# Kernel optimization log

Measured on AMD Instinct MI355X. Metric: run time of the kernel, lower is better.

The kernel has to match this reference:

```python
import jax, jax.numpy as jnp
import numpy as np

SEQ_LEN = 512
EMB_DIM = 2 * SEQ_LEN  # 1024
HIDDEN = 512
NUM_CLASSES = 10
BATCH = 256
VOCAB = 3


def setup_inputs() -> dict:
    key = jax.random.key(0)
    ks = jax.random.split(key, 16)
    def kaiming(k, shape, gain):
        fan_in = shape[0]
        return jax.random.normal(k, shape, dtype=jnp.float32) * (gain / np.sqrt(fan_in))
    tanh_g, sig_g, lin_g = np.sqrt(5.0 / 3.0), 1.0, 1.0
    return {
        "x": jax.random.randint(ks[0], (BATCH, SEQ_LEN), 0, VOCAB),
        "emb": jax.random.normal(ks[1], (VOCAB, EMB_DIM), dtype=jnp.float32),
        "W_gx": kaiming(ks[2], (EMB_DIM, HIDDEN), tanh_g),
        "W_gh": kaiming(ks[3], (HIDDEN, HIDDEN), tanh_g),
        "b_g": jnp.zeros((HIDDEN,), jnp.float32),
        "W_ix": kaiming(ks[4], (EMB_DIM, HIDDEN), sig_g),
        "W_ih": kaiming(ks[5], (HIDDEN, HIDDEN), sig_g),
        "b_i": jnp.zeros((HIDDEN,), jnp.float32),
        "W_fx": kaiming(ks[6], (EMB_DIM, HIDDEN), sig_g),
        "W_fh": kaiming(ks[7], (HIDDEN, HIDDEN), sig_g),
        "b_f": jnp.zeros((HIDDEN,), jnp.float32),
        "W_ox": kaiming(ks[8], (EMB_DIM, HIDDEN), sig_g),
        "W_oh": kaiming(ks[9], (HIDDEN, HIDDEN), sig_g),
        "b_o": jnp.zeros((HIDDEN,), jnp.float32),
        "W_ph": kaiming(ks[10], (HIDDEN, NUM_CLASSES), lin_g),
        "b_p": jnp.zeros((NUM_CLASSES,), jnp.float32),
    }


def reference(x, emb, W_gx, W_gh, b_g, W_ix, W_ih, b_i,
              W_fx, W_fh, b_f, W_ox, W_oh, b_o, W_ph, b_p):
    # Embed all tokens: [B, T, E]
    xe = emb[x]
    B = xe.shape[0]
    # Precompute input projections for all gates once: [T, B, 4H]
    Wx = jnp.concatenate([W_gx, W_ix, W_fx, W_ox], axis=1)  # [E, 4H]
    Wh = jnp.concatenate([W_gh, W_ih, W_fh, W_oh], axis=1)  # [H, 4H]
    b = jnp.concatenate([b_g, b_i, b_f, b_o])               # [4H]
    xg = jnp.einsum('bte,ef->tbf', xe, Wx) + b               # [T, B, 4H]

    H = W_gh.shape[0]

    def step(carry, xg_t):
        h, c = carry
        gates = xg_t + h @ Wh  # [B, 4H]
        g = jnp.tanh(gates[:, 0*H:1*H])
        i = jax.nn.sigmoid(gates[:, 1*H:2*H])
        f = jax.nn.sigmoid(gates[:, 2*H:3*H])
        o = jax.nn.sigmoid(gates[:, 3*H:4*H])
        c = g * i + c * f
        h = jnp.tanh(c) * o
        return (h, c), None

    h0 = jnp.zeros((B, H), xe.dtype)
    c0 = jnp.zeros((B, H), xe.dtype)
    (h_t, _), _ = jax.lax.scan(step, (h0, c0), xg)
    p = h_t @ W_ph + b_p
    return jax.nn.log_softmax(p, axis=1)
```

## Files before the change

kernel.cpp:

```cpp
#include <hip/hip_runtime.h>


typedef __attribute__((ext_vector_type(8))) _Float16 f16x8;
typedef __attribute__((ext_vector_type(4))) float f32x4;
typedef __attribute__((ext_vector_type(4))) unsigned u32x4;
typedef __attribute__((ext_vector_type(2))) unsigned u32x2;

#define NTHR 256
constexpr int T_LEN = 512, EMB = 1024, HID = 512, NCLS = 10;
constexpr int GSIZE = 16;
constexpr int NGRP  = 16;
constexpr int BPG   = 16;
constexpr int UPC   = 32;
constexpr int COLS_PC = 128;
constexpr int NKT = 16;
constexpr int GUNITS  = GSIZE * 128;
constexpr int GSTRIDE = 3 * GUNITS;

__device__ __forceinline__ float sigmf(float x)    { return 1.f / (1.f + __expf(-x)); }
__device__ __forceinline__ float tanhfast(float x) { return 1.f - 2.f / (__expf(2.f * x) + 1.f); }

__device__ __forceinline__ void ld_pair(const u32x4* p, u32x4& a, u32x4& b) {
  asm volatile("global_load_dwordx4 %0, %2, off sc0 sc1\n\t"
               "global_load_dwordx4 %1, %2, off offset:16 sc0 sc1"
               : "=&v"(a), "=&v"(b) : "v"(p) : "memory");
}
__device__ __forceinline__ void wait_vm0() {
  asm volatile("s_waitcnt vmcnt(0)" ::: "memory");
  __builtin_amdgcn_sched_barrier(0);
}
__device__ __forceinline__ void st16(u32x4* p, u32x4 v) {
  asm volatile("global_store_dwordx4 %0, %1, off sc0 sc1" :: "v"(p), "v"(v) : "memory");
}

__global__ __launch_bounds__(NTHR, 1) void lstm_fused(
    const int* __restrict__ xtok, const float* __restrict__ emb,
    const float* __restrict__ Wgx, const float* __restrict__ Wgh, const float* __restrict__ b_g,
    const float* __restrict__ Wix, const float* __restrict__ Wih, const float* __restrict__ b_i,
    const float* __restrict__ Wfx, const float* __restrict__ Wfh, const float* __restrict__ b_f,
    const float* __restrict__ Wox, const float* __restrict__ Woh, const float* __restrict__ b_o,
    const float* __restrict__ Wph, const float* __restrict__ b_p,
    float* __restrict__ out, u32x4* __restrict__ gb)
{
  const int tid  = threadIdx.x;
  const int wv   = tid >> 6;
  const int lane = tid & 63;
  const int q    = lane >> 4;
  const int c    = lane & 15;
  const int wg   = blockIdx.x;
  const int grp  = wg >> 4;
  const int cu   = wg & 15;

  __shared__ __align__(16) _Float16 h_lds[2][BPG * HID];
  __shared__ __align__(16) _Float16 hstw[4][128];
  __shared__ unsigned char xl[BPG][T_LEN];
  __shared__ float projl[3][COLS_PC];
  __shared__ float projp[3][COLS_PC];

  for (int idx = tid; idx < BPG * T_LEN; idx += NTHR) {
    int bl = idx >> 9, tt = idx & (T_LEN - 1);
    xl[bl][tt] = (unsigned char)xtok[(grp * BPG + bl) * T_LEN + tt];
  }

  {
    int cc = tid & 127, half = tid >> 7;
    int w2 = cc >> 5, nt = (cc >> 4) & 1, c2 = cc & 15;
    int gate = nt * 2 + (c2 >> 3);
    int j = cu * UPC + w2 * 8 + (c2 & 7);
    const float* Wx = gate == 0 ? Wgx : gate == 1 ? Wix : gate == 2 ? Wfx : Wox;
    const float* bb = gate == 0 ? b_g : gate == 1 ? b_i : gate == 2 ? b_f : b_o;
    int e0 = half * (EMB / 2);
    for (int v = 0; v < 3; ++v) {
      float s = half ? 0.f : bb[j];
      const float* er = emb + v * EMB + e0;
      const float* wp = Wx + e0 * HID + j;
      #pragma unroll 4
      for (int e = 0; e < EMB / 2; ++e) s = fmaf(er[e], wp[e * HID], s);
      (half ? projp : projl)[v][cc] = s;
    }
  }
  __syncthreads();
  for (int idx = tid; idx < 3 * COLS_PC; idx += NTHR) {
    int v = idx >> 7, cc = idx & 127;
    projl[v][cc] += projp[v][cc];
  }

  f16x8 Bf[2][NKT];
  {
    int g0 = c >> 3;
    int j = cu * UPC + wv * 8 + (c & 7);
    #pragma unroll
    for (int nt = 0; nt < 2; ++nt) {
      int gate = nt * 2 + g0;
      const float* W = gate == 0 ? Wgh : gate == 1 ? Wih : gate == 2 ? Wfh : Woh;
      #pragma unroll
      for (int kt = 0; kt < NKT; ++kt) {
        f16x8 tmp;
        #pragma unroll
        for (int jj = 0; jj < 8; ++jj)
          tmp[jj] = (_Float16)W[(kt * 32 + q * 8 + jj) * HID + j];
        Bf[nt][kt] = tmp;
      }
    }
  }

  float cst[4] = {0.f, 0.f, 0.f, 0.f};
  u32x4* ug = gb + grp * GSTRIDE;
  int br = 0;
  __syncthreads();

  for (int t = 0; t < T_LEN; ++t) {
    const int pl = t & 1;
    if (t > 0) {
      const unsigned tagv = (unsigned)t;
      const u32x4* rb = ug + br * GUNITS;
      u32x4 ua[4], ubv[4];
      for (;;) {
        #pragma unroll
        for (int i = 0; i < 4; ++i)
          ld_pair(rb + (wv * 4 + i) * 128 + 2 * lane, ua[i], ubv[i]);
        wait_vm0();
        bool ok = true;
        #pragma unroll
        for (int i = 0; i < 4; ++i)
          ok = ok && (ua[i][2] == tagv) && (ubv[i][2] == tagv);
        if (__all((int)ok)) break;
        __builtin_amdgcn_s_sleep(1);
      }
      #pragma unroll
      for (int i = 0; i < 4; ++i) {
        int kt = wv * 4 + i;
        u32x2 lo = {ua[i][0], ua[i][1]};
        u32x2 hi = {ubv[i][0], ubv[i][1]};
        *(u32x2*)&h_lds[pl][kt * 512 + lane * 8]     = lo;
        *(u32x2*)&h_lds[pl][kt * 512 + lane * 8 + 4] = hi;
      }
    }
    __syncthreads();

    f32x4 acc0 = {0.f, 0.f, 0.f, 0.f}, acc1 = {0.f, 0.f, 0.f, 0.f};
    if (t > 0) {
      const _Float16* hp = h_lds[pl];
      #pragma unroll
      for (int kt = 0; kt < NKT; ++kt) {
        f16x8 a = *(const f16x8*)(hp + kt * 512 + lane * 8);
        acc0 = __builtin_amdgcn_mfma_f32_16x16x32_f16(a, Bf[0][kt], acc0, 0, 0, 0);
        acc1 = __builtin_amdgcn_mfma_f32_16x16x32_f16(a, Bf[1][kt], acc1, 0, 0, 0);
      }
    }

    bool lo8 = (c < 8);
    #pragma unroll
    for (int r = 0; r < 4; ++r) {
      int bl = q * 4 + r;
      int v = xl[bl][t];
      float p0 = acc0[r] + projl[v][wv * 32 + c];
      float p1 = acc1[r] + projl[v][wv * 32 + 16 + c];
      float p0x = __shfl_xor(p0, 8);
      float p1x = __shfl_xor(p1, 8);
      float gg = lo8 ? p0  : p0x;
      float ii = lo8 ? p0x : p0;
      float ff = lo8 ? p1  : p1x;
      float oo = lo8 ? p1x : p1;
      gg = tanhfast(gg); ii = sigmf(ii); ff = sigmf(ff); oo = sigmf(oo);
      float cn = fmaf(cst[r], ff, gg * ii);
      cst[r] = cn;
      float hv = tanhfast(cn) * oo;
      if (lo8) hstw[wv][bl * 8 + c] = (_Float16)hv;
    }

    int bw = (br + 1 == 3) ? 0 : br + 1;
    if (lane < 32) {
      const unsigned* hw = (const unsigned*)&hstw[wv][0];
      u32x4 pv = {hw[2 * lane], hw[2 * lane + 1], (unsigned)(t + 1), 0u};
      st16(ug + bw * GUNITS + cu * 128 + wv * 32 + lane, pv);
    }
    br = bw;
  }

  if (wv == 0) {
    const u32x4* rb = ug + 2 * GUNITS;
    int kt = lane >> 2, qa = lane & 3;
    const u32x4* p = rb + kt * 128 + 2 * (qa * 16 + cu);
    u32x4 a, b;
    for (;;) {
      ld_pair(p, a, b);
      wait_vm0();
      bool ok = (a[2] == (unsigned)T_LEN) && (b[2] == (unsigned)T_LEN);
      if (__all((int)ok)) break;
      __builtin_amdgcn_s_sleep(1);
    }
    _Float16 hh[8];
    u32x2 lo2 = {a[0], a[1]}, hi2 = {b[0], b[1]};
    __builtin_memcpy(&hh[0], &lo2, 8);
    __builtin_memcpy(&hh[4], &hi2, 8);
    float pc[NCLS];
    #pragma unroll
    for (int k2 = 0; k2 < NCLS; ++k2) pc[k2] = 0.f;
    int jbase = kt * 32 + qa * 8;
    #pragma unroll
    for (int jj = 0; jj < 8; ++jj) {
      float hv = (float)hh[jj];
      const float* wr = Wph + (jbase + jj) * NCLS;
      #pragma unroll
      for (int k2 = 0; k2 < NCLS; ++k2) pc[k2] = fmaf(hv, wr[k2], pc[k2]);
    }
    #pragma unroll
    for (int off = 32; off > 0; off >>= 1) {
      #pragma unroll
      for (int k2 = 0; k2 < NCLS; ++k2) pc[k2] += __shfl_down(pc[k2], off);
    }
    if (lane == 0) {
      float mx = -1e30f;
      #pragma unroll
      for (int k2 = 0; k2 < NCLS; ++k2) { pc[k2] += b_p[k2]; mx = fmaxf(mx, pc[k2]); }
      float se = 0.f;
      #pragma unroll
      for (int k2 = 0; k2 < NCLS; ++k2) se += __expf(pc[k2] - mx);
      float ls = mx + __logf(se);
      int b2 = grp * BPG + cu;
      #pragma unroll
      for (int k2 = 0; k2 < NCLS; ++k2) out[b2 * NCLS + k2] = pc[k2] - ls;
    }
  }
}

extern "C" void kernel_launch(void* const* d_in, const int* in_sizes, int n_in,
                              void* d_out, int out_size, void* d_ws, size_t ws_size,
                              hipStream_t stream) {
  (void)in_sizes; (void)n_in; (void)out_size; (void)ws_size;
  const int*   x   = (const int*)d_in[0];
  const float* emb = (const float*)d_in[1];
  const float* Wgx = (const float*)d_in[2];
  const float* Wgh = (const float*)d_in[3];
  const float* bg  = (const float*)d_in[4];
  const float* Wix = (const float*)d_in[5];
  const float* Wih = (const float*)d_in[6];
  const float* bi  = (const float*)d_in[7];
  const float* Wfx = (const float*)d_in[8];
  const float* Wfh = (const float*)d_in[9];
  const float* bfv = (const float*)d_in[10];
  const float* Wox = (const float*)d_in[11];
  const float* Woh = (const float*)d_in[12];
  const float* bo  = (const float*)d_in[13];
  const float* Wph = (const float*)d_in[14];
  const float* bp  = (const float*)d_in[15];
  float* out = (float*)d_out;

  (void)hipMemsetAsync(d_ws, 0, (size_t)NGRP * GSTRIDE * 16, stream);
  lstm_fused<<<dim3(NGRP * GSIZE), dim3(NTHR), 0, stream>>>(
      x, emb, Wgx, Wgh, bg, Wix, Wih, bi, Wfx, Wfh, bfv,
      Wox, Woh, bo, Wph, bp, out, (u32x4*)d_ws);
}
```

Measured before the change: 1.868 ms.

## Load full hidden state per wave directly from global, drop LDS staging and barrier

Each wave now polls one cheap tag word, then loads all 16 k-tiles of the previous hidden state straight from global memory into registers and feeds them to the MFMAs. This removes the LDS double buffer, the per-step __syncthreads, and the LDS write/read round trip. In exchange each wave issues four times as many global loads per step and holds more registers. The extra traffic goes to cache lines that other workgroups are still writing.

```diff
diff --git a/kernel.cpp b/kernel.cpp
--- a/kernel.cpp
+++ b/kernel.cpp
@@ -4,7 +4,6 @@
 typedef __attribute__((ext_vector_type(8))) _Float16 f16x8;
 typedef __attribute__((ext_vector_type(4))) float f32x4;
 typedef __attribute__((ext_vector_type(4))) unsigned u32x4;
-typedef __attribute__((ext_vector_type(2))) unsigned u32x2;
 
 #define NTHR 256
 constexpr int T_LEN = 512, EMB = 1024, HID = 512, NCLS = 10;
@@ -20,6 +19,12 @@
 __device__ __forceinline__ float sigmf(float x)    { return 1.f / (1.f + __expf(-x)); }
 __device__ __forceinline__ float tanhfast(float x) { return 1.f - 2.f / (__expf(2.f * x) + 1.f); }
 
+__device__ __forceinline__ u32x4 ld16v(const u32x4* p) {
+  u32x4 v;
+  asm volatile("global_load_dwordx4 %0, %1, off sc0 sc1\n\ts_waitcnt vmcnt(0)"
+               : "=v"(v) : "v"(p) : "memory");
+  return v;
+}
 __device__ __forceinline__ void ld_pair(const u32x4* p, u32x4& a, u32x4& b) {
   asm volatile("global_load_dwordx4 %0, %2, off sc0 sc1\n\t"
                "global_load_dwordx4 %1, %2, off offset:16 sc0 sc1"
@@ -51,7 +56,6 @@
   const int grp  = wg >> 4;
   const int cu   = wg & 15;
 
-  __shared__ __align__(16) _Float16 h_lds[2][BPG * HID];
   __shared__ __align__(16) _Float16 hstw[4][128];
   __shared__ unsigned char xl[BPG][T_LEN];
   __shared__ float projl[3][COLS_PC];
@@ -110,40 +114,31 @@
   __syncthreads();
 
   for (int t = 0; t < T_LEN; ++t) {
-    const int pl = t & 1;
+    f32x4 acc0 = {0.f, 0.f, 0.f, 0.f}, acc1 = {0.f, 0.f, 0.f, 0.f};
     if (t > 0) {
       const unsigned tagv = (unsigned)t;
       const u32x4* rb = ug + br * GUNITS;
-      u32x4 ua[4], ubv[4];
+      const u32x4* cp = rb + (lane >> 2) * 128 + (lane & 3) * 32;
+      u32x4 ua[NKT], ub[NKT];
       for (;;) {
+        u32x4 cv = ld16v(cp);
+        if (!__all((int)(cv[2] == tagv))) { __builtin_amdgcn_s_sleep(1); continue; }
         #pragma unroll
-        for (int i = 0; i < 4; ++i)
-          ld_pair(rb + (wv * 4 + i) * 128 + 2 * lane, ua[i], ubv[i]);
+        for (int i = 0; i < NKT; ++i)
+          ld_pair(rb + i * 128 + 2 * lane, ua[i], ub[i]);
         wait_vm0();
         bool ok = true;
         #pragma unroll
-        for (int i = 0; i < 4; ++i)
-          ok = ok && (ua[i][2] == tagv) && (ubv[i][2] == tagv);
+        for (int i = 0; i < NKT; ++i)
+          ok = ok && (ua[i][2] == tagv) && (ub[i][2] == tagv);
         if (__all((int)ok)) break;
         __builtin_amdgcn_s_sleep(1);
       }
       #pragma unroll
-      for (int i = 0; i < 4; ++i) {
-        int kt = wv * 4 + i;
-        u32x2 lo = {ua[i][0], ua[i][1]};
-        u32x2 hi = {ubv[i][0], ubv[i][1]};
-        *(u32x2*)&h_lds[pl][kt * 512 + lane * 8]     = lo;
-        *(u32x2*)&h_lds[pl][kt * 512 + lane * 8 + 4] = hi;
-      }
-    }
-    __syncthreads();
-
-    f32x4 acc0 = {0.f, 0.f, 0.f, 0.f}, acc1 = {0.f, 0.f, 0.f, 0.f};
-    if (t > 0) {
-      const _Float16* hp = h_lds[pl];
-      #pragma unroll
       for (int kt = 0; kt < NKT; ++kt) {
-        f16x8 a = *(const f16x8*)(hp + kt * 512 + lane * 8);
+        u32x4 av = {ua[kt][0], ua[kt][1], ub[kt][0], ub[kt][1]};
+        f16x8 a;
+        __builtin_memcpy(&a, &av, 16);
         acc0 = __builtin_amdgcn_mfma_f32_16x16x32_f16(a, Bf[0][kt], acc0, 0, 0, 0);
         acc1 = __builtin_amdgcn_mfma_f32_16x16x32_f16(a, Bf[1][kt], acc1, 0, 0, 0);
       }
@@ -191,9 +186,8 @@
       __builtin_amdgcn_s_sleep(1);
     }
     _Float16 hh[8];
-    u32x2 lo2 = {a[0], a[1]}, hi2 = {b[0], b[1]};
-    __builtin_memcpy(&hh[0], &lo2, 8);
-    __builtin_memcpy(&hh[4], &hi2, 8);
+    unsigned hw2[4] = {a[0], a[1], b[0], b[1]};
+    __builtin_memcpy(&hh[0], &hw2[0], 16);
     float pc[NCLS];
     #pragma unroll
     for (int k2 = 0; k2 < NCLS; ++k2) pc[k2] = 0.f;
```

Result: slower. 2.659 ms (+42.4%).

## Split batch into 32 groups of 8 rows, two workgroups per CU

Applied to the files above, without the earlier changes.

Halves the batch rows per group (16 to 8) and doubles the number of groups, so 512 workgroups run with launch bounds allowing two per CU. The MFMA still processes 16 rows, but half are zero padding; the inter-workgroup h exchange buffer shrinks, and only the valid rows are polled, stored and used for gate math. The aim is more concurrent recurrence chains, with less exchange traffic and fewer waiters per sync. In exchange, half of each MFMA is wasted work, and register pressure and co-residency of the spin-waiting groups become a concern.

```diff
diff --git a/kernel.cpp b/kernel.cpp
--- a/kernel.cpp
+++ b/kernel.cpp
@@ -9,12 +9,12 @@
 #define NTHR 256
 constexpr int T_LEN = 512, EMB = 1024, HID = 512, NCLS = 10;
 constexpr int GSIZE = 16;
-constexpr int NGRP  = 16;
-constexpr int BPG   = 16;
+constexpr int NGRP  = 32;
+constexpr int BPG   = 8;
 constexpr int UPC   = 32;
 constexpr int COLS_PC = 128;
 constexpr int NKT = 16;
-constexpr int GUNITS  = GSIZE * 128;
+constexpr int GUNITS  = GSIZE * 64;
 constexpr int GSTRIDE = 3 * GUNITS;
 
 __device__ __forceinline__ float sigmf(float x)    { return 1.f / (1.f + __expf(-x)); }
@@ -33,7 +33,7 @@
   asm volatile("global_store_dwordx4 %0, %1, off sc0 sc1" :: "v"(p), "v"(v) : "memory");
 }
 
-__global__ __launch_bounds__(NTHR, 1) void lstm_fused(
+__global__ __launch_bounds__(NTHR, 2) void lstm_fused(
     const int* __restrict__ xtok, const float* __restrict__ emb,
     const float* __restrict__ Wgx, const float* __restrict__ Wgh, const float* __restrict__ b_g,
     const float* __restrict__ Wix, const float* __restrict__ Wih, const float* __restrict__ b_i,
@@ -51,11 +51,17 @@
   const int grp  = wg >> 4;
   const int cu   = wg & 15;
 
-  __shared__ __align__(16) _Float16 h_lds[2][BPG * HID];
-  __shared__ __align__(16) _Float16 hstw[4][128];
+  __shared__ __align__(16) _Float16 h_lds[2][16 * 512];
+  __shared__ __align__(16) _Float16 hstw[4][64];
   __shared__ unsigned char xl[BPG][T_LEN];
   __shared__ float projl[3][COLS_PC];
   __shared__ float projp[3][COLS_PC];
+
+  {
+    unsigned* hz = (unsigned*)&h_lds[0][0];
+    #pragma unroll
+    for (int i = 0; i < 32; ++i) hz[tid + i * NTHR] = 0u;
+  }
 
   for (int idx = tid; idx < BPG * T_LEN; idx += NTHR) {
     int bl = idx >> 9, tt = idx & (T_LEN - 1);
@@ -107,6 +113,8 @@
   float cst[4] = {0.f, 0.f, 0.f, 0.f};
   u32x4* ug = gb + grp * GSTRIDE;
   int br = 0;
+  const int row = c;
+  const bool vrow = (row < 8);
   __syncthreads();
 
   for (int t = 0; t < T_LEN; ++t) {
@@ -116,24 +124,31 @@
       const u32x4* rb = ug + br * GUNITS;
       u32x4 ua[4], ubv[4];
       for (;;) {
-        #pragma unroll
-        for (int i = 0; i < 4; ++i)
-          ld_pair(rb + (wv * 4 + i) * 128 + 2 * lane, ua[i], ubv[i]);
-        wait_vm0();
+        if (vrow) {
+          #pragma unroll
+          for (int i = 0; i < 4; ++i)
+            ld_pair(rb + (wv * 4 + i) * 64 + q * 16 + row * 2, ua[i], ubv[i]);
+          wait_vm0();
+        }
         bool ok = true;
-        #pragma unroll
-        for (int i = 0; i < 4; ++i)
-          ok = ok && (ua[i][2] == tagv) && (ubv[i][2] == tagv);
+        if (vrow) {
+          #pragma unroll
+          for (int i = 0; i < 4; ++i)
+            ok = ok && (ua[i][2] == tagv) && (ubv[i][2] == tagv);
+        }
         if (__all((int)ok)) break;
         __builtin_amdgcn_s_sleep(1);
       }
-      #pragma unroll
-      for (int i = 0; i < 4; ++i) {
-        int kt = wv * 4 + i;
-        u32x2 lo = {ua[i][0], ua[i][1]};
-        u32x2 hi = {ubv[i][0], ubv[i][1]};
-        *(u32x2*)&h_lds[pl][kt * 512 + lane * 8]     = lo;
-        *(u32x2*)&h_lds[pl][kt * 512 + lane * 8 + 4] = hi;
+      if (vrow) {
+        #pragma unroll
+        for (int i = 0; i < 4; ++i) {
+          int kt = wv * 4 + i;
+          u32x2 lo = {ua[i][0], ua[i][1]};
+          u32x2 hi = {ubv[i][0], ubv[i][1]};
+          _Float16* dst = &h_lds[pl][kt * 512 + q * 128 + row * 8];
+          *(u32x2*)dst       = lo;
+          *(u32x2*)(dst + 4) = hi;
+        }
       }
     }
     __syncthreads();
@@ -149,39 +164,41 @@
       }
     }
 
-    bool lo8 = (c < 8);
-    #pragma unroll
-    for (int r = 0; r < 4; ++r) {
-      int bl = q * 4 + r;
-      int v = xl[bl][t];
-      float p0 = acc0[r] + projl[v][wv * 32 + c];
-      float p1 = acc1[r] + projl[v][wv * 32 + 16 + c];
-      float p0x = __shfl_xor(p0, 8);
-      float p1x = __shfl_xor(p1, 8);
-      float gg = lo8 ? p0  : p0x;
-      float ii = lo8 ? p0x : p0;
-      float ff = lo8 ? p1  : p1x;
-      float oo = lo8 ? p1x : p1;
-      gg = tanhfast(gg); ii = sigmf(ii); ff = sigmf(ff); oo = sigmf(oo);
-      float cn = fmaf(cst[r], ff, gg * ii);
-      cst[r] = cn;
-      float hv = tanhfast(cn) * oo;
-      if (lo8) hstw[wv][bl * 8 + c] = (_Float16)hv;
+    if (q < 2) {
+      bool lo8 = (c < 8);
+      #pragma unroll
+      for (int r = 0; r < 4; ++r) {
+        int bl = q * 4 + r;
+        int v = xl[bl][t];
+        float p0 = acc0[r] + projl[v][wv * 32 + c];
+        float p1 = acc1[r] + projl[v][wv * 32 + 16 + c];
+        float p0x = __shfl_xor(p0, 8);
+        float p1x = __shfl_xor(p1, 8);
+        float gg = lo8 ? p0  : p0x;
+        float ii = lo8 ? p0x : p0;
+        float ff = lo8 ? p1  : p1x;
+        float oo = lo8 ? p1x : p1;
+        gg = tanhfast(gg); ii = sigmf(ii); ff = sigmf(ff); oo = sigmf(oo);
+        float cn = fmaf(cst[r], ff, gg * ii);
+        cst[r] = cn;
+        float hv = tanhfast(cn) * oo;
+        if (lo8) hstw[wv][bl * 8 + c] = (_Float16)hv;
+      }
     }
 
     int bw = (br + 1 == 3) ? 0 : br + 1;
-    if (lane < 32) {
+    if (lane < 16) {
       const unsigned* hw = (const unsigned*)&hstw[wv][0];
       u32x4 pv = {hw[2 * lane], hw[2 * lane + 1], (unsigned)(t + 1), 0u};
-      st16(ug + bw * GUNITS + cu * 128 + wv * 32 + lane, pv);
+      st16(ug + bw * GUNITS + cu * 64 + wv * 16 + lane, pv);
     }
     br = bw;
   }
 
-  if (wv == 0) {
+  if (wv == 0 && cu < 8) {
     const u32x4* rb = ug + 2 * GUNITS;
     int kt = lane >> 2, qa = lane & 3;
-    const u32x4* p = rb + kt * 128 + 2 * (qa * 16 + cu);
+    const u32x4* p = rb + kt * 64 + qa * 16 + cu * 2;
     u32x4 a, b;
     for (;;) {
       ld_pair(p, a, b);
@@ -191,9 +208,8 @@
       __builtin_amdgcn_s_sleep(1);
     }
     _Float16 hh[8];
-    u32x2 lo2 = {a[0], a[1]}, hi2 = {b[0], b[1]};
-    __builtin_memcpy(&hh[0], &lo2, 8);
-    __builtin_memcpy(&hh[4], &hi2, 8);
+    unsigned hw2[4] = {a[0], a[1], b[0], b[1]};
+    __builtin_memcpy(&hh[0], &hw2[0], 16);
     float pc[NCLS];
     #pragma unroll
     for (int k2 = 0; k2 < NCLS; ++k2) pc[k2] = 0.f;
```

Result: slower. 2.226 ms (+19.2%).
